# Kernel optimization log

Measured on AMD Instinct MI355X. Metric: run time of the kernel, lower is better.

The kernel has to match this reference:

```python
import jax, jax.numpy as jnp
import numpy as np

C = 96        # d_model
DI = 192      # d_inner = 2*C
N = 16        # d_state
R = 6         # dt_rank = ceil(C/16)
K = 4         # scan directions
B_, H_, W_ = 2, 48, 48


def setup_inputs():
    key = jax.random.key(0)
    ks = jax.random.split(key, 12)
    def rn(k, shape, s=0.02):
        return jax.random.normal(k, shape, jnp.float32) * s
    # S4D-real A init and realistic dt bias (inverse softplus of dt in [1e-3, 1e-1])
    A = jnp.tile(jnp.arange(1, N + 1, dtype=jnp.float32), (K, DI, 1))
    dt = jax.random.uniform(ks[0], (K, DI), jnp.float32, 1e-3, 1e-1)
    inv_softplus_dt = dt + jnp.log(-jnp.expm1(-dt))
    return {
        "x": jax.random.normal(ks[1], (B_, C, H_, W_), jnp.float32),
        "ln1_w": jnp.ones((C,), jnp.float32), "ln1_b": jnp.zeros((C,), jnp.float32),
        "in_proj_w": rn(ks[2], (2 * DI, C)),
        "conv_w": rn(ks[3], (DI, 1, 3, 3), 0.1), "conv_b": jnp.zeros((DI,), jnp.float32),
        "x_proj_w": rn(ks[4], (K, R + 2 * N, DI)),
        "dt_proj_w": rn(ks[5], (K, DI, R), 0.1), "dt_proj_b": inv_softplus_dt,
        "A_log": jnp.log(A), "Ds": jnp.ones((K, DI), jnp.float32),
        "out_norm_w": jnp.ones((DI,), jnp.float32), "out_norm_b": jnp.zeros((DI,), jnp.float32),
        "out_proj_w": rn(ks[6], (C, DI)),
        "ln2_w": jnp.ones((C,), jnp.float32), "ln2_b": jnp.zeros((C,), jnp.float32),
        "fc1_w": rn(ks[7], (C, C)), "fc1_b": jnp.zeros((C,), jnp.float32),
        "fc2_w": rn(ks[8], (C, C)), "fc2_b": jnp.zeros((C,), jnp.float32),
        "proj_w": rn(ks[9], (1, C)), "proj_b": jnp.zeros((1,), jnp.float32),
    }


def _layernorm(x, w, b, eps=1e-5):
    mu = x.mean(-1, keepdims=True)
    var = x.var(-1, keepdims=True)
    return (x - mu) * jax.lax.rsqrt(var + eps) * w + b


def _selective_scan(u, delta, A, Bm, Cm, D):
    # u, delta: (B,K,D,L); A: (K,D,N); Bm, Cm: (B,K,N,L); D: (K,D)
    dA = jnp.exp(jnp.einsum('bkdl,kdn->lbkdn', delta, A))
    dBu = jnp.einsum('bkdl,bknl->lbkdn', delta * u, Bm)
    Ct = jnp.moveaxis(Cm, -1, 0)  # (L,B,K,N)
    h0 = jnp.zeros(dA.shape[1:], u.dtype)
    def step(h, inp):
        dA_t, dBu_t, C_t = inp
        h = dA_t * h + dBu_t
        y = jnp.einsum('bkdn,bkn->bkd', h, C_t)
        return h, y
    _, ys = jax.lax.scan(step, h0, (dA, dBu, Ct))
    y = jnp.moveaxis(ys, 0, -1)  # (B,K,D,L)
    return y + u * D[None, :, :, None]


def _ss2d(x, in_proj_w, conv_w, conv_b, x_proj_w, dt_proj_w, dt_proj_b,
          A_log, Ds, out_norm_w, out_norm_b, out_proj_w):
    Bsz, H, W, _ = x.shape
    L = H * W
    xz = x @ in_proj_w.T                      # (B,H,W,2*DI)
    xh, z = jnp.split(xz, 2, axis=-1)
    xc = xh.transpose(0, 3, 1, 2)             # (B,DI,H,W)
    xc = jax.lax.conv_general_dilated(
        xc, conv_w, (1, 1), ((1, 1), (1, 1)),
        feature_group_count=DI,
        dimension_numbers=('NCHW', 'OIHW', 'NCHW')) + conv_b[None, :, None, None]
    xc = jax.nn.silu(xc)
    # cross-scan: 4 directions (row-major, col-major, and their reverses)
    xf = xc.reshape(Bsz, DI, L)
    xt = xc.transpose(0, 1, 3, 2).reshape(Bsz, DI, L)
    xs2 = jnp.stack([xf, xt], axis=1)
    xs = jnp.concatenate([xs2, jnp.flip(xs2, axis=-1)], axis=1)   # (B,4,DI,L)
    x_dbl = jnp.einsum('bkdl,kcd->bkcl', xs, x_proj_w)
    dts, Bm, Cm = jnp.split(x_dbl, [R, R + N], axis=2)
    delta = jnp.einsum('bkrl,kdr->bkdl', dts, dt_proj_w) + dt_proj_b[None, :, :, None]
    delta = jax.nn.softplus(delta)
    A = -jnp.exp(A_log)
    out_y = _selective_scan(xs, delta, A, Bm, Cm, Ds)             # (B,4,DI,L)
    # cross-merge: undo flips/transposes and sum
    inv_y = jnp.flip(out_y[:, 2:4], axis=-1)
    wh_y = out_y[:, 1].reshape(Bsz, DI, W, H).transpose(0, 1, 3, 2).reshape(Bsz, DI, L)
    invwh_y = inv_y[:, 1].reshape(Bsz, DI, W, H).transpose(0, 1, 3, 2).reshape(Bsz, DI, L)
    y = out_y[:, 0] + inv_y[:, 0] + wh_y + invwh_y                # (B,DI,L)
    y = _layernorm(y.transpose(0, 2, 1), out_norm_w, out_norm_b).reshape(Bsz, H, W, DI)
    y = y * jax.nn.silu(z)
    return y @ out_proj_w.T


def reference(x, ln1_w, ln1_b, in_proj_w, conv_w, conv_b, x_proj_w, dt_proj_w,
              dt_proj_b, A_log, Ds, out_norm_w, out_norm_b, out_proj_w,
              ln2_w, ln2_b, fc1_w, fc1_b, fc2_w, fc2_b, proj_w, proj_b):
    xh = x.transpose(0, 2, 3, 1)   # (B,H,W,C)
    # VSSBlock (pre-norm): x = x + SS2D(LN(x)); x = x + MLP(LN(x))
    h1 = _layernorm(xh, ln1_w, ln1_b)
    xh = xh + _ss2d(h1, in_proj_w, conv_w, conv_b, x_proj_w, dt_proj_w,
                    dt_proj_b, A_log, Ds, out_norm_w, out_norm_b, out_proj_w)
    h2 = _layernorm(xh, ln2_w, ln2_b)
    xh = xh + (jax.nn.gelu(h2 @ fc1_w.T + fc1_b, approximate=False) @ fc2_w.T + fc2_b)
    # 1x1 conv projector + sigmoid
    y = xh @ proj_w.T + proj_b     # (B,H,W,1)
    return jax.nn.sigmoid(y).transpose(0, 3, 1, 2)
```

## Files before the change

### kernel.cpp

```cpp
#include <hip/hip_runtime.h>
#include <cstdint>

static constexpr int LSZ = 2304;
static constexpr int CBS = 96;
static constexpr int DIN = 192;
static constexpr int NST = 16;
static constexpr int HHT = 48;
static constexpr int WWD = 48;
static constexpr int CHN = 16;
static constexpr int CHL = 144;

static constexpr size_t OFF_XCONV = 0;
static constexpr size_t OFF_SILUZ = 884736;
static constexpr size_t OFF_XC    = 1769472;
static constexpr size_t OFF_XCT   = 2654208;
static constexpr size_t OFF_BCT   = 3686400;
static constexpr size_t OFF_DELTA = 4276224;
static constexpr size_t OFF_YK    = 7815168;
static constexpr size_t OFF_WT    = 11796480;

__device__ __forceinline__ float f4get(const float4& v, int i) {
    return i == 0 ? v.x : i == 1 ? v.y : i == 2 ? v.z : v.w;
}

__device__ __forceinline__ float rotadd16(float v) {
    int m;
    m = __builtin_amdgcn_update_dpp(0, __float_as_int(v), 0x128, 0xf, 0xf, false); v += __int_as_float(m);
    m = __builtin_amdgcn_update_dpp(0, __float_as_int(v), 0x124, 0xf, 0xf, false); v += __int_as_float(m);
    m = __builtin_amdgcn_update_dpp(0, __float_as_int(v), 0x122, 0xf, 0xf, false); v += __int_as_float(m);
    m = __builtin_amdgcn_update_dpp(0, __float_as_int(v), 0x121, 0xf, 0xf, false); v += __int_as_float(m);
    return v;
}

__global__ __launch_bounds__(256) void kPrep(const float* __restrict__ Wp,
    const float* __restrict__ Wo, const float* __restrict__ W1,
    const float* __restrict__ W2, float* __restrict__ wt) {
    int e = blockIdx.x * 256 + threadIdx.x;
    if (e < 36864) {
        int cq = e / 1536, rem = e % 1536; int t = rem >> 2, q = rem & 3;
        int c = 4 * cq + q;
        wt[e] = Wp[t * 96 + c];
    } else if (e < 55296) {
        int e2 = e - 36864;
        int dq = e2 / 384, rem = e2 % 384; int tp = rem >> 2, q = rem & 3;
        int d2 = 4 * dq + q;
        wt[e] = Wo[tp * 192 + d2];
    } else if (e < 64512) {
        int e3 = e - 55296;
        int jq = e3 / 384, rem = e3 % 384; int tp = rem >> 2, q = rem & 3;
        int j = 4 * jq + q;
        wt[e] = W1[tp * 96 + j];
    } else if (e < 73728) {
        int e3 = e - 64512;
        int jq = e3 / 384, rem = e3 % 384; int tp = rem >> 2, q = rem & 3;
        int j = 4 * jq + q;
        wt[e] = W2[tp * 96 + j];
    }
}

__global__ __launch_bounds__(768) void kA(const float* __restrict__ x,
    const float* __restrict__ ln1w, const float* __restrict__ ln1b,
    const float* __restrict__ Wt, float* __restrict__ xconv, float* __restrict__ siluz) {
    int blk = blockIdx.x; int b = blk / 144; int s0 = (blk % 144) * 16;
    int tid = threadIdx.x;
    __shared__ float xln[96][20];
    __shared__ float redA[384][17];
    __shared__ float mu16[16], ir16[16];
#pragma unroll
    for (int it = 0; it < 2; ++it) {
        int e = it * 768 + tid; int c = e >> 4, si = e & 15;
        xln[c][si] = x[((size_t)b * CBS + c) * LSZ + s0 + si];
    }
    __syncthreads();
    if (tid < 64) {
        int si = tid & 15, g = tid >> 4;
        float s1 = 0.f, s2 = 0.f;
        for (int c = g; c < 96; c += 4) { float v = xln[c][si]; s1 += v; s2 += v * v; }
        s1 += __shfl_xor(s1, 16); s2 += __shfl_xor(s2, 16);
        s1 += __shfl_xor(s1, 32); s2 += __shfl_xor(s2, 32);
        if (g == 0) {
            float mu = s1 * (1.f / 96.f);
            mu16[si] = mu; ir16[si] = rsqrtf(s2 * (1.f / 96.f) - mu * mu + 1e-5f);
        }
    }
    __syncthreads();
#pragma unroll
    for (int it = 0; it < 2; ++it) {
        int e = it * 768 + tid; int c = e >> 4, si = e & 15;
        xln[c][si] = (xln[c][si] - mu16[si]) * ir16[si] * ln1w[c] + ln1b[c];
    }
    __syncthreads();
    int t = tid % 384, cg = tid / 384;
    float acc[16];
#pragma unroll
    for (int i = 0; i < 16; ++i) acc[i] = 0.f;
    const float4* Wt4 = (const float4*)Wt;
    for (int cq = cg * 12; cq < cg * 12 + 12; ++cq) {
        float4 wv = Wt4[cq * 384 + t];
#pragma unroll
        for (int i = 0; i < 16; ++i) {
            acc[i] = fmaf(wv.x, xln[4 * cq + 0][i],
                     fmaf(wv.y, xln[4 * cq + 1][i],
                     fmaf(wv.z, xln[4 * cq + 2][i],
                     fmaf(wv.w, xln[4 * cq + 3][i], acc[i]))));
        }
    }
    if (cg == 1) {
#pragma unroll
        for (int i = 0; i < 16; ++i) redA[t][i] = acc[i];
    }
    __syncthreads();
    if (cg == 0) {
#pragma unroll
        for (int i = 0; i < 16; ++i) acc[i] += redA[t][i];
        if (t < DIN) {
            size_t base = ((size_t)b * DIN + t) * LSZ + s0;
#pragma unroll
            for (int q = 0; q < 4; ++q) {
                float4 v = make_float4(acc[4 * q], acc[4 * q + 1], acc[4 * q + 2], acc[4 * q + 3]);
                *(float4*)(xconv + base + 4 * q) = v;
            }
        } else {
            int tz = t - DIN;
#pragma unroll
            for (int si = 0; si < 16; ++si) {
                float z = acc[si];
                siluz[((size_t)b * LSZ + s0 + si) * DIN + tz] = z / (1.f + __expf(-z));
            }
        }
    }
}

__global__ __launch_bounds__(256) void kB(const float* __restrict__ xconv,
    const float* __restrict__ cw, const float* __restrict__ cb,
    float* __restrict__ xc, float* __restrict__ xcT) {
    int bd = blockIdx.x;
    int d = bd % DIN;
    int tid = threadIdx.x;
    __shared__ float inp[2304];
    __shared__ float outp[48 * 49];
    const float* src = xconv + (size_t)bd * LSZ;
#pragma unroll
    for (int i = 0; i < 9; ++i) inp[i * 256 + tid] = src[i * 256 + tid];
    float w0 = cw[d * 9 + 0], w1 = cw[d * 9 + 1], w2 = cw[d * 9 + 2];
    float w3 = cw[d * 9 + 3], w4 = cw[d * 9 + 4], w5 = cw[d * 9 + 5];
    float w6 = cw[d * 9 + 6], w7 = cw[d * 9 + 7], w8 = cw[d * 9 + 8];
    float bias = cb[d];
    __syncthreads();
#pragma unroll
    for (int i = 0; i < 9; ++i) {
        int s = i * 256 + tid; int h = s / 48, w = s % 48;
        float acc = bias;
        bool hn = h > 0, hp = h < 47, wn = w > 0, wp = w < 47;
        if (hn) {
            if (wn) acc = fmaf(inp[s - 49], w0, acc);
            acc = fmaf(inp[s - 48], w1, acc);
            if (wp) acc = fmaf(inp[s - 47], w2, acc);
        }
        if (wn) acc = fmaf(inp[s - 1], w3, acc);
        acc = fmaf(inp[s], w4, acc);
        if (wp) acc = fmaf(inp[s + 1], w5, acc);
        if (hp) {
            if (wn) acc = fmaf(inp[s + 47], w6, acc);
            acc = fmaf(inp[s + 48], w7, acc);
            if (wp) acc = fmaf(inp[s + 49], w8, acc);
        }
        float r = acc / (1.f + __expf(-acc));
        xc[(size_t)bd * LSZ + s] = r;
        outp[h * 49 + w] = r;
    }
    __syncthreads();
#pragma unroll
    for (int i = 0; i < 9; ++i) {
        int p = i * 256 + tid;
        int w = p / 48, h = p % 48;
        xcT[(size_t)bd * LSZ + p] = outp[h * 49 + w];
    }
}

__global__ __launch_bounds__(256) void kC(const float* __restrict__ xc,
    const float* __restrict__ xcT, const float* __restrict__ xpw,
    const float* __restrict__ dtw, const float* __restrict__ dtb,
    float* __restrict__ BCt, float* __restrict__ delta) {
    int blk = blockIdx.x; int lt = blk % 36; int k = (blk / 36) & 3; int b = blk / 144;
    int l0 = lt * 64;
    int bk = b * 4 + k;
    __shared__ float xs[DIN][64];
    __shared__ float stage[64][33];
    __shared__ float dtrL[6][64];
    __shared__ float wsh[DIN * 6];
    __shared__ float bshL[DIN];
    const float* src = ((k & 1) ? xcT : xc) + (size_t)b * DIN * LSZ;
    bool fwd = (k < 2);
    int tid = threadIdx.x;
    for (int e = tid; e < 1152; e += 256) wsh[e] = dtw[k * 1152 + e];
    if (tid < DIN) bshL[tid] = dtb[k * DIN + tid];
#pragma unroll
    for (int i = 0; i < 48; ++i) {
        int e = i * 256 + tid; int d = e >> 6, ll = e & 63;
        int l = l0 + ll; int sl = fwd ? l : (LSZ - 1 - l);
        xs[d][ll] = src[(size_t)d * LSZ + sl];
    }
    __syncthreads();
    int c0 = tid >> 6, ll = tid & 63;
    float acc[10];
#pragma unroll
    for (int j = 0; j < 10; ++j) acc[j] = 0.f;
    for (int d0 = 0; d0 < DIN; d0 += 16) {
        float xv[16];
#pragma unroll
        for (int i = 0; i < 16; ++i) xv[i] = xs[d0 + i][ll];
#pragma unroll
        for (int j = 0; j < 10; ++j) {
            int c = j * 4 + c0;
            if (c < 38) {
                const float4* wr = (const float4*)(xpw + ((size_t)(k * 38 + c)) * DIN + d0);
                float4 q0 = wr[0], q1 = wr[1], q2 = wr[2], q3 = wr[3];
                acc[j] += xv[0] * q0.x + xv[1] * q0.y + xv[2] * q0.z + xv[3] * q0.w
                        + xv[4] * q1.x + xv[5] * q1.y + xv[6] * q1.z + xv[7] * q1.w
                        + xv[8] * q2.x + xv[9] * q2.y + xv[10] * q2.z + xv[11] * q2.w
                        + xv[12] * q3.x + xv[13] * q3.y + xv[14] * q3.z + xv[15] * q3.w;
            }
        }
    }
#pragma unroll
    for (int j = 0; j < 10; ++j) {
        int c = j * 4 + c0;
        if (c < 6) {
            dtrL[c][ll] = acc[j];
        } else if (c < 38) {
            int n2 = (c < 22) ? (c - 6) : (16 + c - 22);
            stage[ll][n2] = acc[j];
        }
    }
    __syncthreads();
    float* dst = BCt + ((size_t)bk * LSZ + l0) * 32;
#pragma unroll
    for (int it = 0; it < 8; ++it) {
        int e = it * 256 + tid;
        int l = e >> 5, n2 = e & 31;
        dst[e] = stage[l][n2];
    }
    int dsub = tid >> 6;
    float dr[6];
#pragma unroll
    for (int r = 0; r < 6; ++r) dr[r] = dtrL[r][ll];
    for (int j = 0; j < 48; ++j) {
        int d = j * 4 + dsub;
        float a2 = bshL[d];
#pragma unroll
        for (int r = 0; r < 6; ++r) a2 = fmaf(dr[r], wsh[d * 6 + r], a2);
        float sp = (a2 > 20.f) ? a2 : log1pf(__expf(a2));
        delta[((size_t)bk * DIN + d) * LSZ + l0 + ll] = sp;
    }
}

__global__ __launch_bounds__(256, 4) void kD(const float* __restrict__ delta,
    const float* __restrict__ xc, const float* __restrict__ xcT,
    const float* __restrict__ BCt, const float* __restrict__ A_log, float* __restrict__ yk) {
    int g = blockIdx.x;
    int tid = threadIdx.x;
    int n = tid & 15; int c = tid >> 4;
    int d = g % DIN; int bk = g / DIN; int k = bk & 3; int b = bk >> 2;
    __shared__ float hfinL[256];
    __shared__ float sumdL[16];
    __shared__ float hinL[256];

    float An2 = -__expf(A_log[((size_t)(k * DIN + d)) * NST + n]) * 1.44269504f;
    const float* ub = ((k & 1) ? xcT : xc) + ((size_t)(b * DIN + d)) * LSZ;
    bool fwd = (k < 2);
    int l0 = c * CHL;
    const float* dp = delta + (size_t)g * LSZ + l0;
    const float* up = fwd ? (ub + l0) : (ub + (LSZ - 4) - l0);
    const float* bc = BCt + ((size_t)bk * LSZ + l0) * 32 + n;

    float h = 0.f, sd = 0.f;
    for (int j0 = 0; j0 < CHL; j0 += 4) {
        float4 dv = *(const float4*)(dp + j0);
        float4 uv;
        if (fwd) uv = *(const float4*)(up + j0);
        else { float4 tv = *(const float4*)(up - j0); uv = make_float4(tv.w, tv.z, tv.y, tv.x); }
#pragma unroll
        for (int jj = 0; jj < 4; ++jj) {
            float bn = bc[(j0 + jj) * 32];
            float dl = f4get(dv, jj);
            float da = __builtin_amdgcn_exp2f(dl * An2);
            h = fmaf(da, h, dl * f4get(uv, jj) * bn);
            sd += dl;
        }
    }
    hfinL[tid] = h;
    if (n == 0) sumdL[c] = sd;
    __syncthreads();

    if (tid < 16) {
        float hh = 0.f;
#pragma unroll
        for (int cc = 0; cc < 16; ++cc) {
            hinL[cc * 16 + tid] = hh;
            hh = fmaf(__builtin_amdgcn_exp2f(An2 * sumdL[cc]), hh, hfinL[cc * 16 + tid]);
        }
    }
    __syncthreads();

    h = hinL[tid];
    float* yo = yk + (size_t)g * LSZ + l0 + n;
    for (int m = 0; m < 9; ++m) {
        float ykeep = 0.f;
        for (int q = 0; q < 4; ++q) {
            int j0 = m * 16 + q * 4;
            float4 dv = *(const float4*)(dp + j0);
            float4 uv;
            if (fwd) uv = *(const float4*)(up + j0);
            else { float4 tv = *(const float4*)(up - j0); uv = make_float4(tv.w, tv.z, tv.y, tv.x); }
#pragma unroll
            for (int jj = 0; jj < 4; ++jj) {
                float bn = bc[(j0 + jj) * 32];
                float cn = bc[(j0 + jj) * 32 + 16];
                float dl = f4get(dv, jj);
                float da = __builtin_amdgcn_exp2f(dl * An2);
                h = fmaf(da, h, dl * f4get(uv, jj) * bn);
                float p = rotadd16(h * cn);
                ykeep = (n == q * 4 + jj) ? p : ykeep;
            }
        }
        yo[m * 16] = ykeep;
    }
}

__global__ __launch_bounds__(256) void kM(const float* __restrict__ yk,
    const float* __restrict__ xc, const float* __restrict__ Dsp, float* __restrict__ ym) {
    int blk = blockIdx.x;
    int b = blk / DIN; int d = blk % DIN;
    int tid = threadIdx.x;
    __shared__ float buf[4][48 * 49];
    float Dsum = Dsp[d] + Dsp[DIN + d] + Dsp[2 * DIN + d] + Dsp[3 * DIN + d];
#pragma unroll
    for (int kk = 0; kk < 4; ++kk) {
        const float* src = yk + ((size_t)((b * 4 + kk) * DIN + d)) * LSZ;
#pragma unroll
        for (int i = 0; i < 9; ++i) {
            int s = i * 256 + tid;
            buf[kk][s + s / 48] = src[s];
        }
    }
    __syncthreads();
    const float* xrow = xc + ((size_t)(b * DIN + d)) * LSZ;
    float* dst = ym + ((size_t)blk) * LSZ;
#pragma unroll
    for (int i = 0; i < 9; ++i) {
        int s = i * 256 + tid; int hh = s / 48, ww = s % 48;
        float v0 = buf[0][hh * 49 + ww];
        float v2 = buf[2][(47 - hh) * 49 + (47 - ww)];
        float v1 = buf[1][ww * 49 + hh];
        float v3 = buf[3][(47 - ww) * 49 + (47 - hh)];
        dst[s] = v0 + v2 + v1 + v3 + Dsum * xrow[s];
    }
}

__global__ __launch_bounds__(384) void kEF(const float* __restrict__ ym,
    const float* __restrict__ siluz, const float* __restrict__ x,
    const float* __restrict__ onw, const float* __restrict__ onb,
    const float* __restrict__ WoT,
    const float* __restrict__ l2w, const float* __restrict__ l2b,
    const float* __restrict__ W1T, const float* __restrict__ b1,
    const float* __restrict__ W2T, const float* __restrict__ b2,
    const float* __restrict__ pw, const float* __restrict__ pb, float* __restrict__ out) {
    int blk = blockIdx.x; int b = blk / 144; int s0 = (blk % 144) * 16;
    int tid = threadIdx.x;
    __shared__ float yl[DIN][17];
    __shared__ float xo[96][17];
    __shared__ float aa[96][17];
    __shared__ float red[384][9];
    __shared__ float mu16[16], ir16[16];
#pragma unroll
    for (int it = 0; it < 8; ++it) {
        int e = it * 384 + tid; int d = e >> 4, si = e & 15;
        yl[d][si] = ym[((size_t)(b * DIN + d)) * LSZ + s0 + si];
    }
    __syncthreads();
    if (tid < 64) {
        int si = tid & 15, g = tid >> 4;
        float s1 = 0.f, s2 = 0.f;
        for (int c = g; c < 192; c += 4) { float v = yl[c][si]; s1 += v; s2 += v * v; }
        s1 += __shfl_xor(s1, 16); s2 += __shfl_xor(s2, 16);
        s1 += __shfl_xor(s1, 32); s2 += __shfl_xor(s2, 32);
        if (g == 0) {
            float mu = s1 * (1.f / 192.f);
            mu16[si] = mu; ir16[si] = rsqrtf(s2 * (1.f / 192.f) - mu * mu + 1e-5f);
        }
    }
    __syncthreads();
    {
        int d = tid % 192, sh = tid / 192;
#pragma unroll
        for (int i = 0; i < 8; ++i) {
            int si = sh * 8 + i;
            float v = yl[d][si];
            v = (v - mu16[si]) * ir16[si] * onw[d] + onb[d];
            yl[d][si] = v * siluz[((size_t)b * LSZ + s0 + si) * DIN + d];
        }
    }
    __syncthreads();
    int tp = tid % 96, half = (tid / 96) & 1, kg = tid / 192;
    const float4* WoT4 = (const float4*)WoT;
    const float4* W1T4 = (const float4*)W1T;
    const float4* W2T4 = (const float4*)W2T;
    {
        float acc[8];
#pragma unroll
        for (int i = 0; i < 8; ++i) acc[i] = 0.f;
        for (int dq = kg * 24; dq < kg * 24 + 24; ++dq) {
            float4 wv = WoT4[dq * 96 + tp];
#pragma unroll
            for (int i = 0; i < 8; ++i) {
                acc[i] = fmaf(wv.x, yl[4 * dq + 0][half * 8 + i],
                         fmaf(wv.y, yl[4 * dq + 1][half * 8 + i],
                         fmaf(wv.z, yl[4 * dq + 2][half * 8 + i],
                         fmaf(wv.w, yl[4 * dq + 3][half * 8 + i], acc[i]))));
            }
        }
#pragma unroll
        for (int i = 0; i < 8; ++i) red[tid][i] = acc[i];
    }
    __syncthreads();
    if (tid < 192) {
#pragma unroll
        for (int i = 0; i < 8; ++i) {
            int si = half * 8 + i;
            xo[tp][si] = x[((size_t)b * CBS + tp) * LSZ + s0 + si] + red[tid][i] + red[tid + 192][i];
        }
    }
    __syncthreads();
    if (tid < 64) {
        int si = tid & 15, g = tid >> 4;
        float s1 = 0.f, s2 = 0.f;
        for (int c = g; c < 96; c += 4) { float v = xo[c][si]; s1 += v; s2 += v * v; }
        s1 += __shfl_xor(s1, 16); s2 += __shfl_xor(s2, 16);
        s1 += __shfl_xor(s1, 32); s2 += __shfl_xor(s2, 32);
        if (g == 0) {
            float mu = s1 * (1.f / 96.f);
            mu16[si] = mu; ir16[si] = rsqrtf(s2 * (1.f / 96.f) - mu * mu + 1e-5f);
        }
    }
    __syncthreads();
#pragma unroll
    for (int it = 0; it < 4; ++it) {
        int e = it * 384 + tid; int si = e / 96, cc = e % 96;
        aa[cc][si] = (xo[cc][si] - mu16[si]) * ir16[si] * l2w[cc] + l2b[cc];
    }
    __syncthreads();
    {
        float acc[8];
#pragma unroll
        for (int i = 0; i < 8; ++i) acc[i] = 0.f;
        for (int jq = kg * 12; jq < kg * 12 + 12; ++jq) {
            float4 wv = W1T4[jq * 96 + tp];
#pragma unroll
            for (int i = 0; i < 8; ++i) {
                acc[i] = fmaf(wv.x, aa[4 * jq + 0][half * 8 + i],
                         fmaf(wv.y, aa[4 * jq + 1][half * 8 + i],
                         fmaf(wv.z, aa[4 * jq + 2][half * 8 + i],
                         fmaf(wv.w, aa[4 * jq + 3][half * 8 + i], acc[i]))));
            }
        }
#pragma unroll
        for (int i = 0; i < 8; ++i) red[tid][i] = acc[i];
    }
    __syncthreads();
    if (tid < 192) {
#pragma unroll
        for (int i = 0; i < 8; ++i) {
            float tv = red[tid][i] + red[tid + 192][i] + b1[tp];
            aa[tp][half * 8 + i] = 0.5f * tv * (1.f + erff(tv * 0.70710678118654752f));
        }
    }
    __syncthreads();
    {
        float acc2[8];
#pragma unroll
        for (int i = 0; i < 8; ++i) acc2[i] = 0.f;
        for (int jq = kg * 12; jq < kg * 12 + 12; ++jq) {
            float4 wv = W2T4[jq * 96 + tp];
#pragma unroll
            for (int i = 0; i < 8; ++i) {
                acc2[i] = fmaf(wv.x, aa[4 * jq + 0][half * 8 + i],
                          fmaf(wv.y, aa[4 * jq + 1][half * 8 + i],
                          fmaf(wv.z, aa[4 * jq + 2][half * 8 + i],
                          fmaf(wv.w, aa[4 * jq + 3][half * 8 + i], acc2[i]))));
            }
        }
#pragma unroll
        for (int i = 0; i < 8; ++i) red[tid][i] = acc2[i];
    }
    __syncthreads();
    if (tid < 192) {
#pragma unroll
        for (int i = 0; i < 8; ++i) {
            float xf = xo[tp][half * 8 + i] + red[tid][i] + red[tid + 192][i] + b2[tp];
            aa[tp][half * 8 + i] = xf * pw[tp];
        }
    }
    __syncthreads();
    if (tid < 64) {
        int si = tid & 15, g = tid >> 4;
        float ss = 0.f;
        for (int c = g; c < 96; c += 4) ss += aa[c][si];
        ss += __shfl_xor(ss, 16);
        ss += __shfl_xor(ss, 32);
        if (g == 0)
            out[(size_t)b * LSZ + s0 + si] = 1.f / (1.f + __expf(-(ss + pb[0])));
    }
}

extern "C" void kernel_launch(void* const* d_in, const int* in_sizes, int n_in,
                              void* d_out, int out_size, void* d_ws, size_t ws_size,
                              hipStream_t stream) {
    const float* x    = (const float*)d_in[0];
    const float* ln1w = (const float*)d_in[1];
    const float* ln1b = (const float*)d_in[2];
    const float* Wp   = (const float*)d_in[3];
    const float* cw   = (const float*)d_in[4];
    const float* cb   = (const float*)d_in[5];
    const float* xpw  = (const float*)d_in[6];
    const float* dtw  = (const float*)d_in[7];
    const float* dtb  = (const float*)d_in[8];
    const float* Alog = (const float*)d_in[9];
    const float* Dsp  = (const float*)d_in[10];
    const float* onw  = (const float*)d_in[11];
    const float* onb  = (const float*)d_in[12];
    const float* Wo   = (const float*)d_in[13];
    const float* l2w  = (const float*)d_in[14];
    const float* l2b  = (const float*)d_in[15];
    const float* W1   = (const float*)d_in[16];
    const float* b1   = (const float*)d_in[17];
    const float* W2   = (const float*)d_in[18];
    const float* b2   = (const float*)d_in[19];
    const float* pw   = (const float*)d_in[20];
    const float* pb   = (const float*)d_in[21];

    float* ws    = (float*)d_ws;
    float* xconv = ws + OFF_XCONV;
    float* ym    = ws + OFF_XCONV;
    float* siluz = ws + OFF_SILUZ;
    float* xc    = ws + OFF_XC;
    float* xcT   = ws + OFF_XCT;
    float* BCt   = ws + OFF_BCT;
    float* delta = ws + OFF_DELTA;
    float* yk    = ws + OFF_YK;
    float* wt    = ws + OFF_WT;
    float* WoT   = wt + 36864;
    float* W1T   = wt + 55296;
    float* W2T   = wt + 64512;

    kPrep<<<288, 256, 0, stream>>>(Wp, Wo, W1, W2, wt);
    kA<<<288, 768, 0, stream>>>(x, ln1w, ln1b, wt, xconv, siluz);
    kB<<<384, 256, 0, stream>>>(xconv, cw, cb, xc, xcT);
    kC<<<288, 256, 0, stream>>>(xc, xcT, xpw, dtw, dtb, BCt, delta);
    kD<<<1536, 256, 0, stream>>>(delta, xc, xcT, BCt, Alog, yk);
    kM<<<384, 256, 0, stream>>>(yk, xc, Dsp, ym);
    kEF<<<288, 384, 0, stream>>>(ym, siluz, x, onw, onb, WoT,
                                 l2w, l2b, W1T, b1, W2T, b2, pw, pb, (float*)d_out);
}
```

Baseline: 176.2 us.

## Fuse direction-merge kernel into output kernel, gathering scan outputs directly

Removes the separate merge kernel that summed the four directional scan outputs plus the D skip term into an intermediate buffer. The output kernel now gathers the four directional values (including transposed and reversed indices) and the skip term while loading its tile. This removes one launch and a full write/read round-trip of the merged buffer. The cost is that the transposed-direction loads are strided and uncoalesced.

```diff
diff --git a/kernel.cpp b/kernel.cpp
--- a/kernel.cpp
+++ b/kernel.cpp
@@ -328,37 +328,8 @@
     }
 }
 
-__global__ __launch_bounds__(256) void kM(const float* __restrict__ yk,
-    const float* __restrict__ xc, const float* __restrict__ Dsp, float* __restrict__ ym) {
-    int blk = blockIdx.x;
-    int b = blk / DIN; int d = blk % DIN;
-    int tid = threadIdx.x;
-    __shared__ float buf[4][48 * 49];
-    float Dsum = Dsp[d] + Dsp[DIN + d] + Dsp[2 * DIN + d] + Dsp[3 * DIN + d];
-#pragma unroll
-    for (int kk = 0; kk < 4; ++kk) {
-        const float* src = yk + ((size_t)((b * 4 + kk) * DIN + d)) * LSZ;
-#pragma unroll
-        for (int i = 0; i < 9; ++i) {
-            int s = i * 256 + tid;
-            buf[kk][s + s / 48] = src[s];
-        }
-    }
-    __syncthreads();
-    const float* xrow = xc + ((size_t)(b * DIN + d)) * LSZ;
-    float* dst = ym + ((size_t)blk) * LSZ;
-#pragma unroll
-    for (int i = 0; i < 9; ++i) {
-        int s = i * 256 + tid; int hh = s / 48, ww = s % 48;
-        float v0 = buf[0][hh * 49 + ww];
-        float v2 = buf[2][(47 - hh) * 49 + (47 - ww)];
-        float v1 = buf[1][ww * 49 + hh];
-        float v3 = buf[3][(47 - ww) * 49 + (47 - hh)];
-        dst[s] = v0 + v2 + v1 + v3 + Dsum * xrow[s];
-    }
-}
-
-__global__ __launch_bounds__(384) void kEF(const float* __restrict__ ym,
+__global__ __launch_bounds__(384) void kEF(const float* __restrict__ yk,
+    const float* __restrict__ xc, const float* __restrict__ Dsp,
     const float* __restrict__ siluz, const float* __restrict__ x,
     const float* __restrict__ onw, const float* __restrict__ onb,
     const float* __restrict__ WoT,
@@ -373,10 +344,20 @@
     __shared__ float aa[96][17];
     __shared__ float red[384][9];
     __shared__ float mu16[16], ir16[16];
+    int h0 = s0 / 48, w0 = s0 % 48;
 #pragma unroll
     for (int it = 0; it < 8; ++it) {
         int e = it * 384 + tid; int d = e >> 4, si = e & 15;
-        yl[d][si] = ym[((size_t)(b * DIN + d)) * LSZ + s0 + si];
+        int s = s0 + si;
+        int p = (w0 + si) * 48 + h0;
+        size_t base = ((size_t)(b * 4) * DIN + d) * LSZ;
+        float v0 = yk[base + s];
+        float v1 = yk[base + (size_t)DIN * LSZ + p];
+        float v2 = yk[base + 2 * (size_t)DIN * LSZ + (2303 - s)];
+        float v3 = yk[base + 3 * (size_t)DIN * LSZ + (2303 - p)];
+        float Dsum = Dsp[d] + Dsp[DIN + d] + Dsp[2 * DIN + d] + Dsp[3 * DIN + d];
+        float xcv = xc[((size_t)(b * DIN + d)) * LSZ + s];
+        yl[d][si] = (v0 + v2) + (v1 + v3) + Dsum * xcv;
     }
     __syncthreads();
     if (tid < 64) {
@@ -541,7 +522,6 @@
 
     float* ws    = (float*)d_ws;
     float* xconv = ws + OFF_XCONV;
-    float* ym    = ws + OFF_XCONV;
     float* siluz = ws + OFF_SILUZ;
     float* xc    = ws + OFF_XC;
     float* xcT   = ws + OFF_XCT;
@@ -558,7 +538,6 @@
     kB<<<384, 256, 0, stream>>>(xconv, cw, cb, xc, xcT);
     kC<<<288, 256, 0, stream>>>(xc, xcT, xpw, dtw, dtb, BCt, delta);
     kD<<<1536, 256, 0, stream>>>(delta, xc, xcT, BCt, Alog, yk);
-    kM<<<384, 256, 0, stream>>>(yk, xc, Dsp, ym);
-    kEF<<<288, 384, 0, stream>>>(ym, siluz, x, onw, onb, WoT,
+    kEF<<<288, 384, 0, stream>>>(yk, xc, Dsp, siluz, x, onw, onb, WoT,
                                  l2w, l2b, W1T, b1, W2T, b2, pw, pb, (float*)d_out);
 }
```

New measurement: 186.2 us. 5.7% more time.
